# Optimization experiments

Measured on AMD Instinct MI355X. Metric: run time of the kernel, lower is better.

The kernel has to match this reference:

```python
import jax, jax.numpy as jnp
import numpy as np

B, T, H, V, IN = 128, 1024, 512, 256, 1

def _uniform(key, shape, fan):
    bound = 1.0 / np.sqrt(fan)
    return jax.random.uniform(key, shape, jnp.float32, -bound, bound)

def setup_inputs() -> dict:
    key = jax.random.key(0)
    ks = jax.random.split(key, 11)
    return {
        'x': jax.random.normal(ks[0], (B, T), jnp.float32),
        # PyTorch LSTMCell params: weight_ih [4H, in], weight_hh [4H, H], biases [4H]
        'W_ih1': _uniform(ks[1], (4 * H, IN), H),
        'W_hh1': _uniform(ks[2], (4 * H, H), H),
        'b_ih1': _uniform(ks[3], (4 * H,), H),
        'b_hh1': _uniform(ks[4], (4 * H,), H),
        'W_ih2': _uniform(ks[5], (4 * H, H), H),
        'W_hh2': _uniform(ks[6], (4 * H, H), H),
        'b_ih2': _uniform(ks[7], (4 * H,), H),
        'b_hh2': _uniform(ks[8], (4 * H,), H),
        'W_lin': _uniform(ks[9], (V, H), H),
        'b_lin': _uniform(ks[10], (V,), H),
    }

def _lstm_cell(x, h, c, W_ih, W_hh, b_ih, b_hh):
    # gates in PyTorch order: input, forget, cell(g), output
    g = x @ W_ih.T + b_ih + h @ W_hh.T + b_hh  # [B, 4H]
    i, f, gg, o = jnp.split(g, 4, axis=-1)
    c_new = jax.nn.sigmoid(f) * c + jax.nn.sigmoid(i) * jnp.tanh(gg)
    h_new = jax.nn.sigmoid(o) * jnp.tanh(c_new)
    return h_new, c_new

def reference(x, W_ih1, W_hh1, b_ih1, b_hh1, W_ih2, W_hh2, b_ih2, b_hh2, W_lin, b_lin):
    Bb, Tt = x.shape
    Hh = W_hh1.shape[1]
    xt = x.T[:, :, None]  # [T, B, 1] -- each timestep is a [B,1] chunk

    def step(carry, x_t):
        h1, c1, h2, c2 = carry
        h1, c1 = _lstm_cell(x_t, h1, c1, W_ih1, W_hh1, b_ih1, b_hh1)
        h2, c2 = _lstm_cell(h1, h2, c2, W_ih2, W_hh2, b_ih2, b_hh2)
        return (h1, c1, h2, c2), h2

    z = jnp.zeros((Bb, Hh), x.dtype)
    _, h2_all = jax.lax.scan(step, (z, z, z, z), xt)  # h2_all: [T, B, H]
    # per-step linear + softmax is time-independent -> batch it after the scan
    logits = jnp.einsum('tbh,vh->btv', h2_all, W_lin) + b_lin  # [B, T, V]
    return jax.nn.softmax(logits, axis=-1)
```

## Files before the change

### kernel.cpp

```cpp
#include <hip/hip_runtime.h>
#include <hip/hip_bf16.h>

#define BB 128
#define TT 1024
#define HH 512
#define VV 256
#define NBLK 128

typedef __attribute__((ext_vector_type(8))) short short8;
typedef __attribute__((ext_vector_type(4))) float floatx4;

__device__ __forceinline__ floatx4 mfma16(short8 a, short8 b, floatx4 c) {
    return __builtin_amdgcn_mfma_f32_16x16x32_bf16(a, b, c, 0, 0, 0);
}
__device__ __forceinline__ float sigm(float x) { return 1.0f / (1.0f + __expf(-x)); }
__device__ __forceinline__ float tanh_fast(float x) {
    return 2.0f / (1.0f + __expf(-2.0f * x)) - 1.0f;
}
__device__ __forceinline__ void vmcnt0() {
    asm volatile("s_waitcnt vmcnt(0)" ::: "memory");
}
__device__ __forceinline__ void vm_fence() {
    asm volatile("s_waitcnt vmcnt(0)" ::: "memory");
    __builtin_amdgcn_sched_barrier(0);
}
__device__ __forceinline__ unsigned ald32(const unsigned* p) {
    return __hip_atomic_load(p, __ATOMIC_RELAXED, __HIP_MEMORY_SCOPE_AGENT);
}
__device__ __forceinline__ void ast32(unsigned* p, unsigned v) {
    __hip_atomic_store(p, v, __ATOMIC_RELAXED, __HIP_MEMORY_SCOPE_AGENT);
}
__device__ __forceinline__ short8 ld16_sc1(const __hip_bfloat16* p) {
    short8 v;
    asm volatile("global_load_dwordx4 %0, %1, off sc1" : "=v"(v) : "v"(p));
    return v;
}

__device__ __forceinline__ int poll1w(const unsigned* line, unsigned tgt, int lane,
                                      unsigned* abf) {
    int it = 0;
    for (;;) {
        unsigned v = tgt;
        if (lane < 32) v = ald32(line + lane);
        if (__all((int)(v >= tgt))) return 0;
        if (++it >= (1 << 20)) { ast32(abf, 1u); return 1; }
        if ((it & 1023) == 0 && ald32(abf) != 0u) return 1;
        __builtin_amdgcn_s_sleep(1);
    }
}

__global__ __launch_bounds__(256) void canon(
    const float* __restrict__ x,
    const float* __restrict__ Whh1, const float* __restrict__ Wih2,
    const float* __restrict__ Whh2, const float* __restrict__ Wlin,
    const float* __restrict__ bih1, const float* __restrict__ bhh1,
    const float* __restrict__ bih2, const float* __restrict__ bhh2,
    __hip_bfloat16* __restrict__ Whh1c, __hip_bfloat16* __restrict__ Wih2c,
    __hip_bfloat16* __restrict__ Whh2c, __hip_bfloat16* __restrict__ Wlinc,
    float* __restrict__ bsum1, float* __restrict__ bsum2,
    float* __restrict__ xT)
{
    const int tid = blockIdx.x * 256 + threadIdx.x;
    const int np  = gridDim.x * 256;
    for (int i = tid; i < 2048 * 512; i += np) {
        Whh1c[i] = __float2bfloat16(Whh1[i]);
        Wih2c[i] = __float2bfloat16(Wih2[i]);
        Whh2c[i] = __float2bfloat16(Whh2[i]);
    }
    for (int i = tid; i < 256 * 512; i += np) Wlinc[i] = __float2bfloat16(Wlin[i]);
    for (int i = tid; i < 2048; i += np) {
        bsum1[i] = bih1[i] + bhh1[i];
        bsum2[i] = bih2[i] + bhh2[i];
    }
    for (int i = tid; i < BB * TT; i += np) {
        int b = i >> 10, t = i & 1023;
        xT[t * BB + b] = x[i];
    }
}

__global__ __launch_bounds__(256, 1) void lstm_persist(
    const float* __restrict__ xT,
    const float* __restrict__ Wih1,
    const __hip_bfloat16* __restrict__ Whh1c,
    const float* __restrict__ bsum1,
    const __hip_bfloat16* __restrict__ Wih2c,
    const __hip_bfloat16* __restrict__ Whh2c,
    const float* __restrict__ bsum2,
    unsigned* __restrict__ flags,
    unsigned* __restrict__ h1all,
    unsigned* __restrict__ h2ring,
    __hip_bfloat16* __restrict__ h2slots)
{
    extern __shared__ __hip_bfloat16 lds[];
    __shared__ unsigned s_ab[2][4];

    const int bid   = blockIdx.x;
    const int stage = bid >> 6;
    const int half  = (bid >> 5) & 1;
    const int lb    = bid & 31;
    const int j0    = lb * 16;
    const int b0    = half * 64;
    const int w     = threadIdx.x >> 6;
    const int lane  = threadIdx.x & 63;
    const int q     = lane >> 4, ln = lane & 15;
    const int r0    = b0 + w * 16;

    unsigned* line1  = flags + half * 1024;
    unsigned* line2  = flags + (2 + half) * 1024;
    unsigned* line1c = flags + (4 + half) * 1024;
    unsigned* abf    = flags + 6 * 1024;
    unsigned* myflag  = ((stage == 0) ? line1 : line2) + lb;
    unsigned* myflagc = line1c + lb;

    {
        const __hip_bfloat16* S0 = (stage == 0) ? Whh1c : Wih2c;
        for (int idx = threadIdx.x; idx < 4096; idx += 256) {
            const int g = idx >> 10, kk = (idx >> 6) & 15, l = idx & 63;
            const int lnt = l & 15, qt = l >> 4;
            const size_t src = (size_t)(g * 512 + j0 + lnt) * 512 + kk * 32 + qt * 8;
            *(float4*)(lds + idx * 8) = *(const float4*)(S0 + src);
            if (stage == 1)
                *(float4*)(lds + 32768 + idx * 8) = *(const float4*)(Whh2c + src);
        }
    }
    __syncthreads();

    float wv[4], bs[4];
    #pragma unroll
    for (int g = 0; g < 4; ++g) {
        const int j = g * 512 + j0 + ln;
        if (stage == 0) { wv[g] = Wih1[j]; bs[g] = bsum1[j]; }
        else            { wv[g] = 0.0f;    bs[g] = bsum2[j]; }
    }
    float cre[4] = {0.0f, 0.0f, 0.0f, 0.0f};

    const __hip_bfloat16* h1bf = (const __hip_bfloat16*)h1all;
    const int aoff = (r0 + ln) * HH + q * 8;
    const int jc   = j0 + (ln & ~1);
    const int rA   = (ln & 1) ? 2 : 0;
    const int bA   = r0 + q * 4 + rA;
    const int o0   = (bA * HH + jc) >> 1;
    const int o1   = ((bA + 1) * HH + jc) >> 1;

    for (int t = 0; t < TT; ++t) {
        floatx4 acc[4];
        #pragma unroll
        for (int g = 0; g < 4; ++g) acc[g] = floatx4{0, 0, 0, 0};
        unsigned pk[4];
        int ab = 0;

        if (stage == 0) {
            if (t > 0) ab = poll1w(line1, (unsigned)t, lane, abf);
            asm volatile("" ::: "memory");
            if (!ab) {
                const __hip_bfloat16* hA = h1bf + (size_t)t * 65536;
                float4 xv4 = *(const float4*)(xT + t * BB + r0 + q * 4);
                short8 A0[16];
                #pragma unroll
                for (int kk = 0; kk < 16; ++kk)
                    A0[kk] = *(const short8*)(hA + aoff + kk * 32);
                #pragma unroll
                for (int kk = 0; kk < 16; ++kk) {
                    #pragma unroll
                    for (int g = 0; g < 4; ++g)
                        acc[g] = mfma16(A0[kk],
                            *(const short8*)(lds + ((g * 16 + kk) * 64 + lane) * 8), acc[g]);
                }
                #pragma unroll
                for (int reg = 0; reg < 4; ++reg) {
                    const float xv = ((const float*)&xv4)[reg];
                    float gi = acc[0][reg] + xv * wv[0] + bs[0];
                    float gf = acc[1][reg] + xv * wv[1] + bs[1];
                    float gg = acc[2][reg] + xv * wv[2] + bs[2];
                    float go = acc[3][reg] + xv * wv[3] + bs[3];
                    float cn = sigm(gf) * cre[reg] + sigm(gi) * tanh_fast(gg);
                    cre[reg] = cn;
                    float hn = sigm(go) * tanh_fast(cn);
                    __hip_bfloat16 hb = __float2bfloat16(hn);
                    unsigned short us; __builtin_memcpy(&us, &hb, 2);
                    unsigned mine = us;
                    unsigned other = (unsigned)__shfl_xor((int)mine, 1, 64);
                    pk[reg] = (ln & 1) ? ((other & 0xffffu) | (mine << 16))
                                       : ((mine & 0xffffu) | (other << 16));
                }
                unsigned* dst = h1all + (size_t)(t + 1) * 32768;
                ast32(dst + o0, pk[rA]);
                ast32(dst + o1, pk[rA + 1]);
            }
            vmcnt0();
            if (lane == 0) s_ab[t & 1][w] = (unsigned)ab;
            __syncthreads();
            unsigned bab = s_ab[t & 1][0] | s_ab[t & 1][1] | s_ab[t & 1][2] | s_ab[t & 1][3];
            if (threadIdx.x == 0 && !bab) {
                ast32(myflag,  (unsigned)(t + 1));
                ast32(myflagc, (unsigned)(t + 1));
            }
            if (bab) break;
        } else {
            const unsigned* pp  = (lane < 32) ? (line1c + lane) : (line2 + (lane - 32));
            const unsigned tgtp = (lane < 32) ? (unsigned)(t + 1) : (unsigned)t;
            unsigned vs = ald32(pp);
            unsigned long long bl = __ballot((int)(vs >= tgtp));
            if ((unsigned)bl != 0xffffffffu)
                ab = poll1w(line1c, (unsigned)(t + 1), lane, abf);
            asm volatile("" ::: "memory");
            if (!ab) {
                const __hip_bfloat16* hA = h1bf + (size_t)(t + 1) * 65536;
                short8 A0[16];
                #pragma unroll
                for (int kk = 0; kk < 16; ++kk)
                    A0[kk] = *(const short8*)(hA + aoff + kk * 32);
                #pragma unroll
                for (int kk = 0; kk < 16; ++kk) {
                    #pragma unroll
                    for (int g = 0; g < 4; ++g)
                        acc[g] = mfma16(A0[kk],
                            *(const short8*)(lds + ((g * 16 + kk) * 64 + lane) * 8), acc[g]);
                }
                if (t > 0) {
                    if ((unsigned)(bl >> 32) != 0xffffffffu)
                        ab = poll1w(line2, (unsigned)t, lane, abf);
                    asm volatile("" ::: "memory");
                    if (!ab) {
                        const __hip_bfloat16* hB =
                            (const __hip_bfloat16*)h2ring + (size_t)(t & 3) * 65536;
                        short8 A1[16];
                        #pragma unroll
                        for (int kk = 0; kk < 16; ++kk)
                            A1[kk] = ld16_sc1(hB + aoff + kk * 32);
                        vm_fence();
                        #pragma unroll
                        for (int kk = 0; kk < 16; ++kk) {
                            #pragma unroll
                            for (int g = 0; g < 4; ++g)
                                acc[g] = mfma16(A1[kk],
                                    *(const short8*)(lds + 32768 + ((g * 16 + kk) * 64 + lane) * 8), acc[g]);
                        }
                    }
                }
            }
            if (!ab) {
                #pragma unroll
                for (int reg = 0; reg < 4; ++reg) {
                    float gi = acc[0][reg] + bs[0];
                    float gf = acc[1][reg] + bs[1];
                    float gg = acc[2][reg] + bs[2];
                    float go = acc[3][reg] + bs[3];
                    float cn = sigm(gf) * cre[reg] + sigm(gi) * tanh_fast(gg);
                    cre[reg] = cn;
                    float hn = sigm(go) * tanh_fast(cn);
                    __hip_bfloat16 hb = __float2bfloat16(hn);
                    unsigned short us; __builtin_memcpy(&us, &hb, 2);
                    unsigned mine = us;
                    unsigned other = (unsigned)__shfl_xor((int)mine, 1, 64);
                    pk[reg] = (ln & 1) ? ((other & 0xffffu) | (mine << 16))
                                       : ((mine & 0xffffu) | (other << 16));
                }
                unsigned* dst = h2ring + (size_t)((t + 1) & 3) * 32768;
                ast32(dst + o0, pk[rA]);
                ast32(dst + o1, pk[rA + 1]);
            }
            vmcnt0();
            if (lane == 0) s_ab[t & 1][w] = (unsigned)ab;
            __syncthreads();
            unsigned bab = s_ab[t & 1][0] | s_ab[t & 1][1] | s_ab[t & 1][2] | s_ab[t & 1][3];
            if (threadIdx.x == 0 && !bab) ast32(myflag, (unsigned)(t + 1));
            if (!bab) {
                unsigned* outs = (unsigned*)h2slots;
                outs[(((size_t)bA * TT + t) * HH + jc) >> 1]       = pk[rA];
                outs[(((size_t)(bA + 1) * TT + t) * HH + jc) >> 1] = pk[rA + 1];
            }
            if (bab) break;
        }
    }
}

__global__ __launch_bounds__(256) void lin_softmax(
    const __hip_bfloat16* __restrict__ Wlinc,
    const float* __restrict__ blin,
    float* out)
{
    const __hip_bfloat16* slots = (const __hip_bfloat16*)out;
    const int w = threadIdx.x >> 6;
    const int lane = threadIdx.x & 63;
    const int q = lane >> 4, ln = lane & 15;
    const int r0 = blockIdx.x * 64 + w * 16;

    floatx4 acc[16];
    #pragma unroll
    for (int n = 0; n < 16; ++n) acc[n] = floatx4{0, 0, 0, 0};

    const size_t arow = (size_t)(r0 + ln) * HH + q * 8;
    #pragma unroll 4
    for (int kk = 0; kk < 16; ++kk) {
        short8 a = *(const short8*)(slots + arow + kk * 32);
        #pragma unroll
        for (int n = 0; n < 16; ++n) {
            short8 bf = *(const short8*)(Wlinc + (n * 16 + ln) * HH + kk * 32 + q * 8);
            acc[n] = mfma16(a, bf, acc[n]);
        }
    }

    float bl[16];
    #pragma unroll
    for (int n = 0; n < 16; ++n) bl[n] = blin[n * 16 + ln];

    #pragma unroll
    for (int reg = 0; reg < 4; ++reg) {
        float v[16];
        float mx = -3.4e38f;
        #pragma unroll
        for (int n = 0; n < 16; ++n) {
            v[n] = acc[n][reg] + bl[n];
            mx = fmaxf(mx, v[n]);
        }
        #pragma unroll
        for (int m = 1; m < 16; m <<= 1) mx = fmaxf(mx, __shfl_xor(mx, m));
        float sum = 0.0f;
        #pragma unroll
        for (int n = 0; n < 16; ++n) { v[n] = __expf(v[n] - mx); sum += v[n]; }
        #pragma unroll
        for (int m = 1; m < 16; m <<= 1) sum += __shfl_xor(sum, m);
        const float inv = 1.0f / sum;

        const int r = r0 + q * 4 + reg;
        #pragma unroll
        for (int n = 0; n < 16; ++n)
            out[(size_t)r * VV + n * 16 + ln] = v[n] * inv;
    }
}

extern "C" void kernel_launch(void* const* d_in, const int* in_sizes, int n_in,
                              void* d_out, int out_size, void* d_ws, size_t ws_size,
                              hipStream_t stream)
{
    const float* x     = (const float*)d_in[0];
    const float* W_ih1 = (const float*)d_in[1];
    const float* W_hh1 = (const float*)d_in[2];
    const float* b_ih1 = (const float*)d_in[3];
    const float* b_hh1 = (const float*)d_in[4];
    const float* W_ih2 = (const float*)d_in[5];
    const float* W_hh2 = (const float*)d_in[6];
    const float* b_ih2 = (const float*)d_in[7];
    const float* b_hh2 = (const float*)d_in[8];
    const float* W_lin = (const float*)d_in[9];
    const float* b_lin = (const float*)d_in[10];

    char* p = (char*)d_ws;
    unsigned* flags  = (unsigned*)p;   p += 28672;
    unsigned* h1all  = (unsigned*)p;   p += (size_t)1025 * 131072;
    const size_t zbytes = 28672 + 131072;
    unsigned* h2ring = (unsigned*)p;   p += (size_t)4 * 131072;
    float* bsum1 = (float*)p;          p += 2048 * 4;
    float* bsum2 = (float*)p;          p += 2048 * 4;
    float* xT    = (float*)p;          p += (size_t)BB * TT * 4;
    __hip_bfloat16* Whh1c = (__hip_bfloat16*)p; p += (size_t)2048 * 512 * 2;
    __hip_bfloat16* Wih2c = (__hip_bfloat16*)p; p += (size_t)2048 * 512 * 2;
    __hip_bfloat16* Whh2c = (__hip_bfloat16*)p; p += (size_t)2048 * 512 * 2;
    __hip_bfloat16* Wlinc = (__hip_bfloat16*)p; p += (size_t)256 * 512 * 2;

    hipMemsetAsync(d_ws, 0, zbytes, stream);

    canon<<<dim3(512), dim3(256), 0, stream>>>(
        x, W_hh1, W_ih2, W_hh2, W_lin, b_ih1, b_hh1, b_ih2, b_hh2,
        Whh1c, Wih2c, Whh2c, Wlinc, bsum1, bsum2, xT);

    const int smem_bytes = 131072;
    (void)hipFuncSetAttribute((const void*)lstm_persist,
                              hipFuncAttributeMaxDynamicSharedMemorySize, smem_bytes);

    lstm_persist<<<dim3(NBLK), dim3(256), smem_bytes, stream>>>(
        xT, W_ih1, Whh1c, bsum1, Wih2c, Whh2c, bsum2,
        flags, h1all, h2ring, (__hip_bfloat16*)d_out);

    lin_softmax<<<dim3((TT * BB) / 64), dim3(256), 0, stream>>>(
        Wlinc, b_lin, (float*)d_out);
}
```

Baseline: 8.563 ms.

## Poll global flags from one wave and replicate flag lines across blocks

Only wave 0 of each block now polls the global step flags. It then releases the other three waves through LDS 'go' counters, so four waves no longer each hammer the same global cache lines. Each producer writes its flag into four replicated flag lines, and each block reads the replica picked by lb&3, which spreads polling traffic across more lines. The layer-2 wait for h2 is moved after the h1 MFMA phase so every wave can see it through LDS. The cost is extra flag stores per step, spin loops on LDS, and a larger zeroed flag region.

```diff
diff --git a/kernel.cpp b/kernel.cpp
--- a/kernel.cpp
+++ b/kernel.cpp
@@ -24,11 +24,21 @@
     asm volatile("s_waitcnt vmcnt(0)" ::: "memory");
     __builtin_amdgcn_sched_barrier(0);
 }
+__device__ __forceinline__ void cfence() {
+    asm volatile("" ::: "memory");
+    __builtin_amdgcn_sched_barrier(0);
+}
 __device__ __forceinline__ unsigned ald32(const unsigned* p) {
     return __hip_atomic_load(p, __ATOMIC_RELAXED, __HIP_MEMORY_SCOPE_AGENT);
 }
 __device__ __forceinline__ void ast32(unsigned* p, unsigned v) {
     __hip_atomic_store(p, v, __ATOMIC_RELAXED, __HIP_MEMORY_SCOPE_AGENT);
+}
+__device__ __forceinline__ unsigned ldsld(const unsigned* p) {
+    return __hip_atomic_load(p, __ATOMIC_RELAXED, __HIP_MEMORY_SCOPE_WORKGROUP);
+}
+__device__ __forceinline__ void ldsst(unsigned* p, unsigned v) {
+    __hip_atomic_store(p, v, __ATOMIC_RELAXED, __HIP_MEMORY_SCOPE_WORKGROUP);
 }
 __device__ __forceinline__ short8 ld16_sc1(const __hip_bfloat16* p) {
     short8 v;
@@ -47,6 +57,13 @@
         if ((it & 1023) == 0 && ald32(abf) != 0u) return 1;
         __builtin_amdgcn_s_sleep(1);
     }
+}
+__device__ __forceinline__ int spin_go(const unsigned* g, unsigned tgt, unsigned* abf) {
+    int it = 0;
+    while (ldsld(g) < tgt) {
+        if (++it >= (1 << 22)) { ast32(abf, 1u); return 1; }
+    }
+    return 0;
 }
 
 __global__ __launch_bounds__(256) void canon(
@@ -93,6 +110,7 @@
 {
     extern __shared__ __hip_bfloat16 lds[];
     __shared__ unsigned s_ab[2][4];
+    __shared__ unsigned go1[8], go2[8];
 
     const int bid   = blockIdx.x;
     const int stage = bid >> 6;
@@ -104,13 +122,12 @@
     const int lane  = threadIdx.x & 63;
     const int q     = lane >> 4, ln = lane & 15;
     const int r0    = b0 + w * 16;
-
-    unsigned* line1  = flags + half * 1024;
-    unsigned* line2  = flags + (2 + half) * 1024;
-    unsigned* line1c = flags + (4 + half) * 1024;
-    unsigned* abf    = flags + 6 * 1024;
-    unsigned* myflag  = ((stage == 0) ? line1 : line2) + lb;
-    unsigned* myflagc = line1c + lb;
+    const int rp    = lb & 3;
+
+    unsigned* l1line  = flags + rp * 1024 + half * 32;
+    unsigned* l2line  = flags + (4 + rp) * 1024 + half * 32;
+    unsigned* l1cline = flags + (8 + rp) * 1024 + half * 32;
+    unsigned* abf     = flags + 12 * 1024;
 
     {
         const __hip_bfloat16* S0 = (stage == 0) ? Whh1c : Wih2c;
@@ -123,6 +140,7 @@
                 *(float4*)(lds + 32768 + idx * 8) = *(const float4*)(Whh2c + src);
         }
     }
+    if (threadIdx.x < 8) { go1[threadIdx.x] = 0u; go2[threadIdx.x] = 0u; }
     __syncthreads();
 
     float wv[4], bs[4];
@@ -150,8 +168,13 @@
         int ab = 0;
 
         if (stage == 0) {
-            if (t > 0) ab = poll1w(line1, (unsigned)t, lane, abf);
-            asm volatile("" ::: "memory");
+            if (w == 0) {
+                if (t > 0) ab = poll1w(l1line, (unsigned)t, lane, abf);
+                ldsst(&go1[t & 7], (unsigned)(t + 1));
+            } else if (t > 0) {
+                ab = spin_go(&go1[t & 7], (unsigned)(t + 1), abf);
+            }
+            cfence();
             if (!ab) {
                 const __hip_bfloat16* hA = h1bf + (size_t)t * 65536;
                 float4 xv4 = *(const float4*)(xT + t * BB + r0 + q * 4);
@@ -192,18 +215,30 @@
             __syncthreads();
             unsigned bab = s_ab[t & 1][0] | s_ab[t & 1][1] | s_ab[t & 1][2] | s_ab[t & 1][3];
             if (threadIdx.x == 0 && !bab) {
-                ast32(myflag,  (unsigned)(t + 1));
-                ast32(myflagc, (unsigned)(t + 1));
+                #pragma unroll
+                for (int r = 0; r < 4; ++r) {
+                    ast32(flags + r * 1024 + half * 32 + lb,       (unsigned)(t + 1));
+                    ast32(flags + (8 + r) * 1024 + half * 32 + lb, (unsigned)(t + 1));
+                }
             }
             if (bab) break;
         } else {
-            const unsigned* pp  = (lane < 32) ? (line1c + lane) : (line2 + (lane - 32));
-            const unsigned tgtp = (lane < 32) ? (unsigned)(t + 1) : (unsigned)t;
-            unsigned vs = ald32(pp);
-            unsigned long long bl = __ballot((int)(vs >= tgtp));
-            if ((unsigned)bl != 0xffffffffu)
-                ab = poll1w(line1c, (unsigned)(t + 1), lane, abf);
-            asm volatile("" ::: "memory");
+            unsigned h2ok = 1u;
+            if (w == 0) {
+                const unsigned* pp  = (lane < 32) ? (l1cline + lane)
+                                                  : (l2line + (lane - 32));
+                const unsigned tgtp = (lane < 32) ? (unsigned)(t + 1) : (unsigned)t;
+                unsigned vs = ald32(pp);
+                unsigned long long bl = __ballot((int)(vs >= tgtp));
+                unsigned h1ok = ((unsigned)bl == 0xffffffffu);
+                h2ok = ((unsigned)(bl >> 32) == 0xffffffffu);
+                if (!h1ok) ab |= poll1w(l1cline, (unsigned)(t + 1), lane, abf);
+                ldsst(&go1[t & 7], (unsigned)(t + 1));
+                if (h2ok) ldsst(&go2[t & 7], (unsigned)(t + 1));
+            } else {
+                ab |= spin_go(&go1[t & 7], (unsigned)(t + 1), abf);
+            }
+            cfence();
             if (!ab) {
                 const __hip_bfloat16* hA = h1bf + (size_t)(t + 1) * 65536;
                 short8 A0[16];
@@ -217,25 +252,31 @@
                         acc[g] = mfma16(A0[kk],
                             *(const short8*)(lds + ((g * 16 + kk) * 64 + lane) * 8), acc[g]);
                 }
-                if (t > 0) {
-                    if ((unsigned)(bl >> 32) != 0xffffffffu)
-                        ab = poll1w(line2, (unsigned)t, lane, abf);
-                    asm volatile("" ::: "memory");
-                    if (!ab) {
-                        const __hip_bfloat16* hB =
-                            (const __hip_bfloat16*)h2ring + (size_t)(t & 3) * 65536;
-                        short8 A1[16];
+            }
+            if (t > 0) {
+                if (w == 0) {
+                    if (!h2ok) {
+                        ab |= poll1w(l2line, (unsigned)t, lane, abf);
+                        ldsst(&go2[t & 7], (unsigned)(t + 1));
+                    }
+                } else {
+                    ab |= spin_go(&go2[t & 7], (unsigned)(t + 1), abf);
+                }
+                cfence();
+                if (!ab) {
+                    const __hip_bfloat16* hB =
+                        (const __hip_bfloat16*)h2ring + (size_t)(t & 3) * 65536;
+                    short8 A1[16];
+                    #pragma unroll
+                    for (int kk = 0; kk < 16; ++kk)
+                        A1[kk] = ld16_sc1(hB + aoff + kk * 32);
+                    vm_fence();
+                    #pragma unroll
+                    for (int kk = 0; kk < 16; ++kk) {
                         #pragma unroll
-                        for (int kk = 0; kk < 16; ++kk)
-                            A1[kk] = ld16_sc1(hB + aoff + kk * 32);
-                        vm_fence();
-                        #pragma unroll
-                        for (int kk = 0; kk < 16; ++kk) {
-                            #pragma unroll
-                            for (int g = 0; g < 4; ++g)
-                                acc[g] = mfma16(A1[kk],
-                                    *(const short8*)(lds + 32768 + ((g * 16 + kk) * 64 + lane) * 8), acc[g]);
-                        }
+                        for (int g = 0; g < 4; ++g)
+                            acc[g] = mfma16(A1[kk],
+                                *(const short8*)(lds + 32768 + ((g * 16 + kk) * 64 + lane) * 8), acc[g]);
                     }
                 }
             }
@@ -264,7 +305,11 @@
             if (lane == 0) s_ab[t & 1][w] = (unsigned)ab;
             __syncthreads();
             unsigned bab = s_ab[t & 1][0] | s_ab[t & 1][1] | s_ab[t & 1][2] | s_ab[t & 1][3];
-            if (threadIdx.x == 0 && !bab) ast32(myflag, (unsigned)(t + 1));
+            if (threadIdx.x == 0 && !bab) {
+                #pragma unroll
+                for (int r = 0; r < 4; ++r)
+                    ast32(flags + (4 + r) * 1024 + half * 32 + lb, (unsigned)(t + 1));
+            }
             if (!bab) {
                 unsigned* outs = (unsigned*)h2slots;
                 outs[(((size_t)bA * TT + t) * HH + jc) >> 1]       = pk[rA];
@@ -347,9 +392,9 @@
     const float* b_lin = (const float*)d_in[10];
 
     char* p = (char*)d_ws;
-    unsigned* flags  = (unsigned*)p;   p += 28672;
+    unsigned* flags  = (unsigned*)p;   p += 65536;
     unsigned* h1all  = (unsigned*)p;   p += (size_t)1025 * 131072;
-    const size_t zbytes = 28672 + 131072;
+    const size_t zbytes = 65536 + 131072;
     unsigned* h2ring = (unsigned*)p;   p += (size_t)4 * 131072;
     float* bsum1 = (float*)p;          p += 2048 * 4;
     float* bsum2 = (float*)p;          p += 2048 * 4;
```

Result: no change. 8.654 ms (+1.1%).

## Halve persistent LSTM grid by processing both batch halves per block

Applied to the files above, without the earlier changes.

The persistent recurrent kernel drops from 128 to 64 blocks. Each block now handles both batch halves in sequence within a timestep, keeping per-half cell state and flags, so the LDS weight tile is shared across both halves. This cuts the number of participating CUs and the cross-block flag traffic, but it serialises twice the work per block on the critical path. The combined stage-2 poll ballot fast path is also replaced by separate poll calls.

```diff
diff --git a/kernel.cpp b/kernel.cpp
--- a/kernel.cpp
+++ b/kernel.cpp
@@ -5,7 +5,7 @@
 #define TT 1024
 #define HH 512
 #define VV 256
-#define NBLK 128
+#define NBLK 64
 
 typedef __attribute__((ext_vector_type(8))) short short8;
 typedef __attribute__((ext_vector_type(4))) float floatx4;
@@ -22,6 +22,10 @@
 }
 __device__ __forceinline__ void vm_fence() {
     asm volatile("s_waitcnt vmcnt(0)" ::: "memory");
+    __builtin_amdgcn_sched_barrier(0);
+}
+__device__ __forceinline__ void cfence() {
+    asm volatile("" ::: "memory");
     __builtin_amdgcn_sched_barrier(0);
 }
 __device__ __forceinline__ unsigned ald32(const unsigned* p) {
@@ -95,22 +99,17 @@
     __shared__ unsigned s_ab[2][4];
 
     const int bid   = blockIdx.x;
-    const int stage = bid >> 6;
-    const int half  = (bid >> 5) & 1;
+    const int stage = bid >> 5;
     const int lb    = bid & 31;
     const int j0    = lb * 16;
-    const int b0    = half * 64;
     const int w     = threadIdx.x >> 6;
     const int lane  = threadIdx.x & 63;
     const int q     = lane >> 4, ln = lane & 15;
-    const int r0    = b0 + w * 16;
-
-    unsigned* line1  = flags + half * 1024;
-    unsigned* line2  = flags + (2 + half) * 1024;
-    unsigned* line1c = flags + (4 + half) * 1024;
-    unsigned* abf    = flags + 6 * 1024;
-    unsigned* myflag  = ((stage == 0) ? line1 : line2) + lb;
-    unsigned* myflagc = line1c + lb;
+
+    unsigned* line1h[2]  = {flags,            flags + 1024};
+    unsigned* line2h[2]  = {flags + 2 * 1024, flags + 3 * 1024};
+    unsigned* line1ch[2] = {flags + 4 * 1024, flags + 5 * 1024};
+    unsigned* abf        = flags + 6 * 1024;
 
     {
         const __hip_bfloat16* S0 = (stage == 0) ? Whh1c : Wih2c;
@@ -132,102 +131,108 @@
         if (stage == 0) { wv[g] = Wih1[j]; bs[g] = bsum1[j]; }
         else            { wv[g] = 0.0f;    bs[g] = bsum2[j]; }
     }
-    float cre[4] = {0.0f, 0.0f, 0.0f, 0.0f};
+    float cre[2][4] = {{0.f, 0.f, 0.f, 0.f}, {0.f, 0.f, 0.f, 0.f}};
 
     const __hip_bfloat16* h1bf = (const __hip_bfloat16*)h1all;
-    const int aoff = (r0 + ln) * HH + q * 8;
-    const int jc   = j0 + (ln & ~1);
-    const int rA   = (ln & 1) ? 2 : 0;
-    const int bA   = r0 + q * 4 + rA;
-    const int o0   = (bA * HH + jc) >> 1;
-    const int o1   = ((bA + 1) * HH + jc) >> 1;
-
-    for (int t = 0; t < TT; ++t) {
-        floatx4 acc[4];
-        #pragma unroll
-        for (int g = 0; g < 4; ++g) acc[g] = floatx4{0, 0, 0, 0};
-        unsigned pk[4];
-        int ab = 0;
-
-        if (stage == 0) {
-            if (t > 0) ab = poll1w(line1, (unsigned)t, lane, abf);
-            asm volatile("" ::: "memory");
-            if (!ab) {
-                const __hip_bfloat16* hA = h1bf + (size_t)t * 65536;
-                float4 xv4 = *(const float4*)(xT + t * BB + r0 + q * 4);
-                short8 A0[16];
-                #pragma unroll
-                for (int kk = 0; kk < 16; ++kk)
-                    A0[kk] = *(const short8*)(hA + aoff + kk * 32);
-                #pragma unroll
-                for (int kk = 0; kk < 16; ++kk) {
-                    #pragma unroll
-                    for (int g = 0; g < 4; ++g)
-                        acc[g] = mfma16(A0[kk],
-                            *(const short8*)(lds + ((g * 16 + kk) * 64 + lane) * 8), acc[g]);
-                }
-                #pragma unroll
-                for (int reg = 0; reg < 4; ++reg) {
-                    const float xv = ((const float*)&xv4)[reg];
-                    float gi = acc[0][reg] + xv * wv[0] + bs[0];
-                    float gf = acc[1][reg] + xv * wv[1] + bs[1];
-                    float gg = acc[2][reg] + xv * wv[2] + bs[2];
-                    float go = acc[3][reg] + xv * wv[3] + bs[3];
-                    float cn = sigm(gf) * cre[reg] + sigm(gi) * tanh_fast(gg);
-                    cre[reg] = cn;
-                    float hn = sigm(go) * tanh_fast(cn);
-                    __hip_bfloat16 hb = __float2bfloat16(hn);
-                    unsigned short us; __builtin_memcpy(&us, &hb, 2);
-                    unsigned mine = us;
-                    unsigned other = (unsigned)__shfl_xor((int)mine, 1, 64);
-                    pk[reg] = (ln & 1) ? ((other & 0xffffu) | (mine << 16))
-                                       : ((mine & 0xffffu) | (other << 16));
-                }
-                unsigned* dst = h1all + (size_t)(t + 1) * 32768;
-                ast32(dst + o0, pk[rA]);
-                ast32(dst + o1, pk[rA + 1]);
-            }
-            vmcnt0();
-            if (lane == 0) s_ab[t & 1][w] = (unsigned)ab;
-            __syncthreads();
-            unsigned bab = s_ab[t & 1][0] | s_ab[t & 1][1] | s_ab[t & 1][2] | s_ab[t & 1][3];
-            if (threadIdx.x == 0 && !bab) {
-                ast32(myflag,  (unsigned)(t + 1));
-                ast32(myflagc, (unsigned)(t + 1));
-            }
-            if (bab) break;
-        } else {
-            const unsigned* pp  = (lane < 32) ? (line1c + lane) : (line2 + (lane - 32));
-            const unsigned tgtp = (lane < 32) ? (unsigned)(t + 1) : (unsigned)t;
-            unsigned vs = ald32(pp);
-            unsigned long long bl = __ballot((int)(vs >= tgtp));
-            if ((unsigned)bl != 0xffffffffu)
-                ab = poll1w(line1c, (unsigned)(t + 1), lane, abf);
-            asm volatile("" ::: "memory");
-            if (!ab) {
-                const __hip_bfloat16* hA = h1bf + (size_t)(t + 1) * 65536;
-                short8 A0[16];
-                #pragma unroll
-                for (int kk = 0; kk < 16; ++kk)
-                    A0[kk] = *(const short8*)(hA + aoff + kk * 32);
-                #pragma unroll
-                for (int kk = 0; kk < 16; ++kk) {
-                    #pragma unroll
-                    for (int g = 0; g < 4; ++g)
-                        acc[g] = mfma16(A0[kk],
-                            *(const short8*)(lds + ((g * 16 + kk) * 64 + lane) * 8), acc[g]);
-                }
-                if (t > 0) {
-                    if ((unsigned)(bl >> 32) != 0xffffffffu)
-                        ab = poll1w(line2, (unsigned)t, lane, abf);
-                    asm volatile("" ::: "memory");
+    const int jc = j0 + (ln & ~1);
+    const int rA = (ln & 1) ? 2 : 0;
+    int aoffh[2], o0h[2], o1h[2], bAh[2], xoffh[2];
+    #pragma unroll
+    for (int h = 0; h < 2; ++h) {
+        const int r0 = h * 64 + w * 16;
+        aoffh[h] = (r0 + ln) * HH + q * 8;
+        const int bA = r0 + q * 4 + rA;
+        bAh[h]  = bA;
+        o0h[h]  = (bA * HH + jc) >> 1;
+        o1h[h]  = ((bA + 1) * HH + jc) >> 1;
+        xoffh[h] = r0 + q * 4;
+    }
+
+    int dead = 0;
+    for (int t = 0; t < TT && !dead; ++t) {
+        #pragma unroll
+        for (int h = 0; h < 2; ++h) {
+            floatx4 acc[4];
+            #pragma unroll
+            for (int g = 0; g < 4; ++g) acc[g] = floatx4{0, 0, 0, 0};
+            unsigned pk[4];
+            int ab = 0;
+            const int k = (2 * t + h) & 1;
+
+            if (stage == 0) {
+                if (t > 0) ab = poll1w(line1h[h], (unsigned)t, lane, abf);
+                cfence();
+                if (!ab) {
+                    const __hip_bfloat16* hA = h1bf + (size_t)t * 65536;
+                    float4 xv4 = *(const float4*)(xT + t * BB + xoffh[h]);
+                    short8 A0[16];
+                    #pragma unroll
+                    for (int kk = 0; kk < 16; ++kk)
+                        A0[kk] = *(const short8*)(hA + aoffh[h] + kk * 32);
+                    #pragma unroll
+                    for (int kk = 0; kk < 16; ++kk) {
+                        #pragma unroll
+                        for (int g = 0; g < 4; ++g)
+                            acc[g] = mfma16(A0[kk],
+                                *(const short8*)(lds + ((g * 16 + kk) * 64 + lane) * 8), acc[g]);
+                    }
+                    #pragma unroll
+                    for (int reg = 0; reg < 4; ++reg) {
+                        const float xv = ((const float*)&xv4)[reg];
+                        float gi = acc[0][reg] + xv * wv[0] + bs[0];
+                        float gf = acc[1][reg] + xv * wv[1] + bs[1];
+                        float gg = acc[2][reg] + xv * wv[2] + bs[2];
+                        float go = acc[3][reg] + xv * wv[3] + bs[3];
+                        float cn = sigm(gf) * cre[h][reg] + sigm(gi) * tanh_fast(gg);
+                        cre[h][reg] = cn;
+                        float hn = sigm(go) * tanh_fast(cn);
+                        __hip_bfloat16 hb = __float2bfloat16(hn);
+                        unsigned short us; __builtin_memcpy(&us, &hb, 2);
+                        unsigned mine = us;
+                        unsigned other = (unsigned)__shfl_xor((int)mine, 1, 64);
+                        pk[reg] = (ln & 1) ? ((other & 0xffffu) | (mine << 16))
+                                           : ((mine & 0xffffu) | (other << 16));
+                    }
+                    unsigned* dst = h1all + (size_t)(t + 1) * 32768;
+                    ast32(dst + o0h[h], pk[rA]);
+                    ast32(dst + o1h[h], pk[rA + 1]);
+                }
+                vmcnt0();
+                if (lane == 0) s_ab[k][w] = (unsigned)ab;
+                __syncthreads();
+                unsigned bab = s_ab[k][0] | s_ab[k][1] | s_ab[k][2] | s_ab[k][3];
+                if (threadIdx.x == 0 && !bab) {
+                    ast32(line1h[h] + lb,  (unsigned)(t + 1));
+                    ast32(line1ch[h] + lb, (unsigned)(t + 1));
+                }
+                if (bab) { dead = 1; }
+            } else {
+                ab = poll1w(line1ch[h], (unsigned)(t + 1), lane, abf);
+                cfence();
+                if (!ab) {
+                    const __hip_bfloat16* hA = h1bf + (size_t)(t + 1) * 65536;
+                    short8 A0[16];
+                    #pragma unroll
+                    for (int kk = 0; kk < 16; ++kk)
+                        A0[kk] = *(const short8*)(hA + aoffh[h] + kk * 32);
+                    #pragma unroll
+                    for (int kk = 0; kk < 16; ++kk) {
+                        #pragma unroll
+                        for (int g = 0; g < 4; ++g)
+                            acc[g] = mfma16(A0[kk],
+                                *(const short8*)(lds + ((g * 16 + kk) * 64 + lane) * 8), acc[g]);
+                    }
+                }
+                if (t > 0 && !ab) {
+                    ab = poll1w(line2h[h], (unsigned)t, lane, abf);
+                    cfence();
                     if (!ab) {
                         const __hip_bfloat16* hB =
                             (const __hip_bfloat16*)h2ring + (size_t)(t & 3) * 65536;
                         short8 A1[16];
                         #pragma unroll
                         for (int kk = 0; kk < 16; ++kk)
-                            A1[kk] = ld16_sc1(hB + aoff + kk * 32);
+                            A1[kk] = ld16_sc1(hB + aoffh[h] + kk * 32);
                         vm_fence();
                         #pragma unroll
                         for (int kk = 0; kk < 16; ++kk) {
@@ -238,39 +243,40 @@
                         }
                     }
                 }
+                if (!ab) {
+                    #pragma unroll
+                    for (int reg = 0; reg < 4; ++reg) {
+                        float gi = acc[0][reg] + bs[0];
+                        float gf = acc[1][reg] + bs[1];
+                        float gg = acc[2][reg] + bs[2];
+                        float go = acc[3][reg] + bs[3];
+                        float cn = sigm(gf) * cre[h][reg] + sigm(gi) * tanh_fast(gg);
+                        cre[h][reg] = cn;
+                        float hn = sigm(go) * tanh_fast(cn);
+                        __hip_bfloat16 hb = __float2bfloat16(hn);
+                        unsigned short us; __builtin_memcpy(&us, &hb, 2);
+                        unsigned mine = us;
+                        unsigned other = (unsigned)__shfl_xor((int)mine, 1, 64);
+                        pk[reg] = (ln & 1) ? ((other & 0xffffu) | (mine << 16))
+                                           : ((mine & 0xffffu) | (other << 16));
+                    }
+                    unsigned* dst = h2ring + (size_t)((t + 1) & 3) * 32768;
+                    ast32(dst + o0h[h], pk[rA]);
+                    ast32(dst + o1h[h], pk[rA + 1]);
+                }
+                vmcnt0();
+                if (lane == 0) s_ab[k][w] = (unsigned)ab;
+                __syncthreads();
+                unsigned bab = s_ab[k][0] | s_ab[k][1] | s_ab[k][2] | s_ab[k][3];
+                if (threadIdx.x == 0 && !bab)
+                    ast32(line2h[h] + lb, (unsigned)(t + 1));
+                if (!bab) {
+                    unsigned* outs = (unsigned*)h2slots;
+                    const int bA = bAh[h];
+                    outs[(((size_t)bA * TT + t) * HH + jc) >> 1]       = pk[rA];
+                    outs[(((size_t)(bA + 1) * TT + t) * HH + jc) >> 1] = pk[rA + 1];
+                } else { dead = 1; }
             }
-            if (!ab) {
-                #pragma unroll
-                for (int reg = 0; reg < 4; ++reg) {
-                    float gi = acc[0][reg] + bs[0];
-                    float gf = acc[1][reg] + bs[1];
-                    float gg = acc[2][reg] + bs[2];
-                    float go = acc[3][reg] + bs[3];
-                    float cn = sigm(gf) * cre[reg] + sigm(gi) * tanh_fast(gg);
-                    cre[reg] = cn;
-                    float hn = sigm(go) * tanh_fast(cn);
-                    __hip_bfloat16 hb = __float2bfloat16(hn);
-                    unsigned short us; __builtin_memcpy(&us, &hb, 2);
-                    unsigned mine = us;
-                    unsigned other = (unsigned)__shfl_xor((int)mine, 1, 64);
-                    pk[reg] = (ln & 1) ? ((other & 0xffffu) | (mine << 16))
-                                       : ((mine & 0xffffu) | (other << 16));
-                }
-                unsigned* dst = h2ring + (size_t)((t + 1) & 3) * 32768;
-                ast32(dst + o0, pk[rA]);
-                ast32(dst + o1, pk[rA + 1]);
-            }
-            vmcnt0();
-            if (lane == 0) s_ab[t & 1][w] = (unsigned)ab;
-            __syncthreads();
-            unsigned bab = s_ab[t & 1][0] | s_ab[t & 1][1] | s_ab[t & 1][2] | s_ab[t & 1][3];
-            if (threadIdx.x == 0 && !bab) ast32(myflag, (unsigned)(t + 1));
-            if (!bab) {
-                unsigned* outs = (unsigned*)h2slots;
-                outs[(((size_t)bA * TT + t) * HH + jc) >> 1]       = pk[rA];
-                outs[(((size_t)(bA + 1) * TT + t) * HH + jc) >> 1] = pk[rA + 1];
-            }
-            if (bab) break;
         }
     }
 }
```

Measured after the change: 16.80 ms. 1.96x slower.
